# Kernel tuning notes

Measured on AMD Instinct MI355X. Metric: run time of the kernel, lower is better.

## Reference

```python
import jax, jax.numpy as jnp
import numpy as np

LATENT = 64
COND = 768
HEADS = 8
R = 8           # LoRA rank
SCALING = 1.0   # lora_alpha / r
SCALE = (LATENT / HEADS) ** -0.5


def _lora_linear(x, W, b, A, B):
    # loralib-style: y = x W^T + b + scaling * (x A^T) B^T
    return x @ W.T + b + SCALING * ((x @ A.T) @ B.T)


def setup_inputs() -> dict:
    key = jax.random.key(0)
    ks = jax.random.split(key, 20)
    B, C, H, W_ = 16, LATENT, 64, 64
    L = 77
    z = jax.random.normal(ks[0], (B, C, H, W_), dtype=jnp.float32)
    cond = jax.random.normal(ks[1], (B, L, COND), dtype=jnp.float32)

    def lin(k, out_d, in_d):
        k1, k2, k3 = jax.random.split(k, 3)
        W = jax.random.normal(k1, (out_d, in_d), dtype=jnp.float32) * 0.02
        b = jnp.zeros((out_d,), dtype=jnp.float32)
        A = jax.random.normal(k2, (R, in_d), dtype=jnp.float32) * 0.02
        Bm = jax.random.normal(k3, (out_d, R), dtype=jnp.float32) * 0.02
        return W, b, A, Bm

    Wq, bq, Aq, Bq = lin(ks[2], LATENT, LATENT)
    Wk, bk, Ak, Bk = lin(ks[3], LATENT, COND)
    Wv, bv, Av, Bv = lin(ks[4], LATENT, COND)
    Wo, bo, Ao, Bo = lin(ks[5], LATENT, LATENT)
    return dict(z=z, cond=cond,
                Wq=Wq, bq=bq, Aq=Aq, Bq=Bq,
                Wk=Wk, bk=bk, Ak=Ak, Bk=Bk,
                Wv=Wv, bv=bv, Av=Av, Bv=Bv,
                Wo=Wo, bo=bo, Ao=Ao, Bo=Bo)


def reference(z, cond, Wq, bq, Aq, Bq, Wk, bk, Ak, Bk, Wv, bv, Av, Bv, Wo, bo, Ao, Bo):
    B, C, H, W_ = z.shape
    hw = H * W_
    dh = C // HEADS
    z_flat = z.transpose(0, 2, 3, 1).reshape(B, hw, C)  # [B, hw, C]

    q = _lora_linear(z_flat, Wq, bq, Aq, Bq)   # [B, hw, C]
    k = _lora_linear(cond, Wk, bk, Ak, Bk)     # [B, L, C]
    v = _lora_linear(cond, Wv, bv, Av, Bv)     # [B, L, C]

    q = q.reshape(B, hw, HEADS, dh).transpose(0, 2, 1, 3)  # [B, h, hw, dh]
    k = k.reshape(B, -1, HEADS, dh).transpose(0, 2, 1, 3)  # [B, h, L, dh]
    v = v.reshape(B, -1, HEADS, dh).transpose(0, 2, 1, 3)

    dots = jnp.einsum('bhqd,bhkd->bhqk', q, k) * SCALE  # [B, h, hw, L]
    attn = jax.nn.softmax(dots, axis=-1)
    out = jnp.einsum('bhqk,bhkd->bhqd', attn, v)        # [B, h, hw, dh]
    out = out.transpose(0, 2, 1, 3).reshape(B, hw, C)
    out = _lora_linear(out, Wo, bo, Ao, Bo)
    return out.reshape(B, H, W_, C).transpose(0, 3, 1, 2)  # [B, C, H, W]
```

## Files before the change

### kernel.cpp

```cpp
#include <hip/hip_runtime.h>


#define HW   4096
#define CHN  64
#define LSEQ 77
#define CD   768
#define NB   16

#define OFF_WQ 0
#define OFF_WK 4096
#define OFF_WV 53248
#define OFF_WO 102400
#define OFF_K  106496
#define OFF_V  185344

#define QF 0.51011784563163f

__global__ __launch_bounds__(256) void prep_weights(
    const float* __restrict__ Wq, const float* __restrict__ Aq, const float* __restrict__ Bq,
    const float* __restrict__ Wk, const float* __restrict__ Ak, const float* __restrict__ Bk,
    const float* __restrict__ Wv, const float* __restrict__ Av, const float* __restrict__ Bv,
    const float* __restrict__ Wo, const float* __restrict__ Ao, const float* __restrict__ Bo,
    float* __restrict__ ws) {
  int idx = blockIdx.x * 256 + threadIdx.x;
  const float *W, *A, *Bm;
  float* out;
  int in_d, local;
  float scale = 1.0f;
  if (idx < 4096)        { W = Wq; A = Aq; Bm = Bq; out = ws + OFF_WQ; in_d = 64;  local = idx; scale = QF; }
  else if (idx < 53248)  { W = Wk; A = Ak; Bm = Bk; out = ws + OFF_WK; in_d = 768; local = idx - 4096; }
  else if (idx < 102400) { W = Wv; A = Av; Bm = Bv; out = ws + OFF_WV; in_d = 768; local = idx - 53248; }
  else                   { W = Wo; A = Ao; Bm = Bo; out = ws + OFF_WO; in_d = 64;  local = idx - 102400; }
  int co = local & 63;
  int c  = local >> 6;
  float val = W[co * in_d + c];
  #pragma unroll
  for (int r = 0; r < 8; r++) val += Bm[co * 8 + r] * A[r * in_d + c];
  out[local] = val * scale;
}

__global__ __launch_bounds__(512, 4) void kvproj2(
    const float* __restrict__ cond,
    const float* __restrict__ wkT,
    const float* __restrict__ wvT,
    const float* __restrict__ bk, const float* __restrict__ bv,
    float* __restrict__ kbuf,
    float* __restrict__ vbuf) {
  int kv = blockIdx.y;
  int t  = threadIdx.x;
  int w  = __builtin_amdgcn_readfirstlane(t >> 6);
  int co = t & 63;
  int row = blockIdx.x * 8 + w;
  const float* wT = kv ? wvT : wkT;
  const float* xr = cond + row * CD;
  float acc = (kv ? bv : bk)[co];
  #pragma unroll 8
  for (int c4 = 0; c4 < CD / 4; c4++) {
    float4 xv = *(const float4*)(xr + 4 * c4);
    acc = fmaf(xv.x, wT[(4 * c4 + 0) * 64 + co], acc);
    acc = fmaf(xv.y, wT[(4 * c4 + 1) * 64 + co], acc);
    acc = fmaf(xv.z, wT[(4 * c4 + 2) * 64 + co], acc);
    acc = fmaf(xv.w, wT[(4 * c4 + 3) * 64 + co], acc);
  }
  (kv ? vbuf : kbuf)[row * 64 + co] = acc;
}

__global__ __launch_bounds__(256, 2) void megattn(
    const float* __restrict__ z,
    const float* __restrict__ wqT,
    const float* __restrict__ bq,
    const float* __restrict__ kbuf,
    const float* __restrict__ vbuf,
    const float* __restrict__ woT,
    const float* __restrict__ bo,
    float* __restrict__ out) {
  __shared__ float smem[LSEQ * 64 * 2];
  int b  = blockIdx.y;
  int p0 = blockIdx.x * 128;
  int t  = threadIdx.x;
  int h  = t >> 5;
  int pl = t & 31;

  float* ks = smem;
  float* vs = smem + LSEQ * 64;
  {
    const float4* ksrc = (const float4*)(kbuf + b * LSEQ * 64);
    const float4* vsrc = (const float4*)(vbuf + b * LSEQ * 64);
    float4* kd = (float4*)ks;
    float4* vd = (float4*)vs;
    for (int i = t; i < LSEQ * 16; i += 256) { kd[i] = ksrc[i]; vd[i] = vsrc[i]; }
  }

  float qr[4][8];
  {
    const float4 b0 = *(const float4*)(bq + 8 * h);
    const float4 b1 = *(const float4*)(bq + 8 * h + 4);
    #pragma unroll
    for (int i = 0; i < 4; i++) {
      qr[i][0] = b0.x * QF; qr[i][1] = b0.y * QF; qr[i][2] = b0.z * QF; qr[i][3] = b0.w * QF;
      qr[i][4] = b1.x * QF; qr[i][5] = b1.y * QF; qr[i][6] = b1.z * QF; qr[i][7] = b1.w * QF;
    }
  }
  const float* zb = z + b * (CHN * HW) + p0 + pl;
  #pragma unroll 4
  for (int c = 0; c < 64; c++) {
    float4 w0 = *(const float4*)(wqT + c * 64 + 8 * h);
    float4 w1 = *(const float4*)(wqT + c * 64 + 8 * h + 4);
    float zv[4];
    #pragma unroll
    for (int i = 0; i < 4; i++) zv[i] = zb[c * HW + 32 * i];
    #pragma unroll
    for (int i = 0; i < 4; i++) {
      qr[i][0] = fmaf(zv[i], w0.x, qr[i][0]);
      qr[i][1] = fmaf(zv[i], w0.y, qr[i][1]);
      qr[i][2] = fmaf(zv[i], w0.z, qr[i][2]);
      qr[i][3] = fmaf(zv[i], w0.w, qr[i][3]);
      qr[i][4] = fmaf(zv[i], w1.x, qr[i][4]);
      qr[i][5] = fmaf(zv[i], w1.y, qr[i][5]);
      qr[i][6] = fmaf(zv[i], w1.z, qr[i][6]);
      qr[i][7] = fmaf(zv[i], w1.w, qr[i][7]);
    }
  }
  __syncthreads();

  float acc[4][8];
  float li[4];
  #pragma unroll
  for (int i = 0; i < 4; i++) {
    li[i] = 0.f;
    #pragma unroll
    for (int d = 0; d < 8; d++) acc[i][d] = 0.f;
  }
  #pragma unroll 2
  for (int j = 0; j < LSEQ; j++) {
    float4 k0 = *(const float4*)(ks + j * 64 + 8 * h);
    float4 k1 = *(const float4*)(ks + j * 64 + 8 * h + 4);
    float4 v0 = *(const float4*)(vs + j * 64 + 8 * h);
    float4 v1 = *(const float4*)(vs + j * 64 + 8 * h + 4);
    #pragma unroll
    for (int i = 0; i < 4; i++) {
      float s = qr[i][0] * k0.x;
      s = fmaf(qr[i][1], k0.y, s);
      s = fmaf(qr[i][2], k0.z, s);
      s = fmaf(qr[i][3], k0.w, s);
      s = fmaf(qr[i][4], k1.x, s);
      s = fmaf(qr[i][5], k1.y, s);
      s = fmaf(qr[i][6], k1.z, s);
      s = fmaf(qr[i][7], k1.w, s);
      float e = __builtin_amdgcn_exp2f(s);
      li[i] += e;
      acc[i][0] = fmaf(e, v0.x, acc[i][0]);
      acc[i][1] = fmaf(e, v0.y, acc[i][1]);
      acc[i][2] = fmaf(e, v0.z, acc[i][2]);
      acc[i][3] = fmaf(e, v0.w, acc[i][3]);
      acc[i][4] = fmaf(e, v1.x, acc[i][4]);
      acc[i][5] = fmaf(e, v1.y, acc[i][5]);
      acc[i][6] = fmaf(e, v1.z, acc[i][6]);
      acc[i][7] = fmaf(e, v1.w, acc[i][7]);
    }
  }
  __syncthreads();

  float* ao = smem;
  #pragma unroll
  for (int i = 0; i < 4; i++) {
    float inv = 1.0f / li[i];
    int p = pl + 32 * i;
    #pragma unroll
    for (int d = 0; d < 8; d++) ao[p * 65 + 8 * h + d] = acc[i][d] * inv;
  }
  __syncthreads();

  int q2 = t & 127;
  int chalf = __builtin_amdgcn_readfirstlane((t >> 7) & 1);
  float acc2[32];
  #pragma unroll
  for (int j2 = 0; j2 < 32; j2++) acc2[j2] = bo[chalf * 32 + j2];
  const float* aor = ao + q2 * 65;
  #pragma unroll 4
  for (int c = 0; c < 64; c++) {
    float xv = aor[c];
    const float* wr = woT + c * 64 + chalf * 32;
    #pragma unroll
    for (int j2 = 0; j2 < 32; j2++) acc2[j2] = fmaf(xv, wr[j2], acc2[j2]);
  }
  float* ob = out + b * (CHN * HW) + p0 + q2;
  #pragma unroll
  for (int j2 = 0; j2 < 32; j2++) ob[(chalf * 32 + j2) * HW] = acc2[j2];
}

extern "C" void kernel_launch(void* const* d_in, const int* in_sizes, int n_in,
                              void* d_out, int out_size, void* d_ws, size_t ws_size,
                              hipStream_t stream) {
  const float* z    = (const float*)d_in[0];
  const float* cond = (const float*)d_in[1];
  const float* Wq = (const float*)d_in[2];  const float* bq = (const float*)d_in[3];
  const float* Aq = (const float*)d_in[4];  const float* Bq = (const float*)d_in[5];
  const float* Wk = (const float*)d_in[6];  const float* bk = (const float*)d_in[7];
  const float* Ak = (const float*)d_in[8];  const float* Bk = (const float*)d_in[9];
  const float* Wv = (const float*)d_in[10]; const float* bv = (const float*)d_in[11];
  const float* Av = (const float*)d_in[12]; const float* Bv = (const float*)d_in[13];
  const float* Wo = (const float*)d_in[14]; const float* bo = (const float*)d_in[15];
  const float* Ao = (const float*)d_in[16]; const float* Bo = (const float*)d_in[17];
  float* ws  = (float*)d_ws;
  float* out = (float*)d_out;

  prep_weights<<<416, 256, 0, stream>>>(Wq, Aq, Bq, Wk, Ak, Bk, Wv, Av, Bv, Wo, Ao, Bo, ws);
  kvproj2<<<dim3(154, 2), 512, 0, stream>>>(cond, ws + OFF_WK, ws + OFF_WV, bk, bv,
                                            ws + OFF_K, ws + OFF_V);
  megattn<<<dim3(32, 16), 256, 0, stream>>>(z, ws + OFF_WQ, bq, ws + OFF_K, ws + OFF_V,
                                            ws + OFF_WO, bo, out);
}
```

Baseline: 169.0 us.

## Split K/V projection reduction across waves and reuse weights over four rows

The K/V projection kernel now stages four cond rows in shared memory and splits the 768-long reduction into four chunks, one per wave. Each thread loads a weight once and applies it to four rows, with a shared-memory reduction at the end. The intent is to cut redundant weight reads and shorten each thread's serial FMA chain, so more blocks run with more parallelism. The cost is extra shared memory, two barriers and a small reduction step.

```diff
diff --git a/kernel.cpp b/kernel.cpp
--- a/kernel.cpp
+++ b/kernel.cpp
@@ -39,30 +39,61 @@
   out[local] = val * scale;
 }
 
-__global__ __launch_bounds__(512, 4) void kvproj2(
+__global__ __launch_bounds__(256) void kvproj4(
     const float* __restrict__ cond,
     const float* __restrict__ wkT,
     const float* __restrict__ wvT,
     const float* __restrict__ bk, const float* __restrict__ bv,
     float* __restrict__ kbuf,
     float* __restrict__ vbuf) {
+  __shared__ float xs[4 * CD];
+  __shared__ float red[4][4][64];
   int kv = blockIdx.y;
+  int r0 = blockIdx.x * 4;
   int t  = threadIdx.x;
-  int w  = __builtin_amdgcn_readfirstlane(t >> 6);
   int co = t & 63;
-  int row = blockIdx.x * 8 + w;
-  const float* wT = kv ? wvT : wkT;
-  const float* xr = cond + row * CD;
-  float acc = (kv ? bv : bk)[co];
-  #pragma unroll 8
-  for (int c4 = 0; c4 < CD / 4; c4++) {
-    float4 xv = *(const float4*)(xr + 4 * c4);
-    acc = fmaf(xv.x, wT[(4 * c4 + 0) * 64 + co], acc);
-    acc = fmaf(xv.y, wT[(4 * c4 + 1) * 64 + co], acc);
-    acc = fmaf(xv.z, wT[(4 * c4 + 2) * 64 + co], acc);
-    acc = fmaf(xv.w, wT[(4 * c4 + 3) * 64 + co], acc);
-  }
-  (kv ? vbuf : kbuf)[row * 64 + co] = acc;
+  int q  = __builtin_amdgcn_readfirstlane(t >> 6);
+
+  {
+    const float4* src = (const float4*)(cond + r0 * CD);
+    float4* dst = (float4*)xs;
+    #pragma unroll
+    for (int i = 0; i < 3; i++) dst[t + 256 * i] = src[t + 256 * i];
+  }
+  __syncthreads();
+
+  const float* wT = (kv ? wvT : wkT) + q * 192 * 64 + co;
+  const float4* xs4 = (const float4*)xs;
+  float acc0 = 0.f, acc1 = 0.f, acc2 = 0.f, acc3 = 0.f;
+  #pragma unroll 4
+  for (int c4 = 0; c4 < 48; c4++) {
+    float w0 = wT[(4 * c4 + 0) * 64];
+    float w1 = wT[(4 * c4 + 1) * 64];
+    float w2 = wT[(4 * c4 + 2) * 64];
+    float w3 = wT[(4 * c4 + 3) * 64];
+    float4 x0 = xs4[0 * 192 + q * 48 + c4];
+    float4 x1 = xs4[1 * 192 + q * 48 + c4];
+    float4 x2 = xs4[2 * 192 + q * 48 + c4];
+    float4 x3 = xs4[3 * 192 + q * 48 + c4];
+    acc0 = fmaf(x0.x, w0, acc0); acc0 = fmaf(x0.y, w1, acc0);
+    acc0 = fmaf(x0.z, w2, acc0); acc0 = fmaf(x0.w, w3, acc0);
+    acc1 = fmaf(x1.x, w0, acc1); acc1 = fmaf(x1.y, w1, acc1);
+    acc1 = fmaf(x1.z, w2, acc1); acc1 = fmaf(x1.w, w3, acc1);
+    acc2 = fmaf(x2.x, w0, acc2); acc2 = fmaf(x2.y, w1, acc2);
+    acc2 = fmaf(x2.z, w2, acc2); acc2 = fmaf(x2.w, w3, acc2);
+    acc3 = fmaf(x3.x, w0, acc3); acc3 = fmaf(x3.y, w1, acc3);
+    acc3 = fmaf(x3.z, w2, acc3); acc3 = fmaf(x3.w, w3, acc3);
+  }
+  red[q][0][co] = acc0;
+  red[q][1][co] = acc1;
+  red[q][2][co] = acc2;
+  red[q][3][co] = acc3;
+  __syncthreads();
+
+  int lr = t >> 6;
+  float val = (kv ? bv : bk)[co]
+            + red[0][lr][co] + red[1][lr][co] + red[2][lr][co] + red[3][lr][co];
+  (kv ? vbuf : kbuf)[(r0 + lr) * 64 + co] = val;
 }
 
 __global__ __launch_bounds__(256, 2) void megattn(
@@ -206,7 +237,7 @@
   float* out = (float*)d_out;
 
   prep_weights<<<416, 256, 0, stream>>>(Wq, Aq, Bq, Wk, Ak, Bk, Wv, Av, Bv, Wo, Ao, Bo, ws);
-  kvproj2<<<dim3(154, 2), 512, 0, stream>>>(cond, ws + OFF_WK, ws + OFF_WV, bk, bv,
+  kvproj4<<<dim3(308, 2), 256, 0, stream>>>(cond, ws + OFF_WK, ws + OFF_WV, bk, bv,
                                             ws + OFF_K, ws + OFF_V);
   megattn<<<dim3(32, 16), 256, 0, stream>>>(z, ws + OFF_WQ, bq, ws + OFF_K, ws + OFF_V,
                                             ws + OFF_WO, bo, out);
```

Result: faster. 147.2 us (-12.9%).

## Split K/V projection reduction across waves with LDS partial-sum reduction

Applied to the files above, without the earlier changes.

Rewrites the K/V projection kernel so each block handles 4 rows, stages the condition rows in shared memory, and splits the 768-long reduction across 16 thread groups that each reuse a float4 weight load across four rows. Partial sums are combined through a shared-memory reduction before adding the bias. This targets the long serial dependency chain and per-thread scalar weight loads of the old one-row-per-wave kernel, and it adds block synchronisation and extra shared memory in exchange.

```diff
diff --git a/kernel.cpp b/kernel.cpp
--- a/kernel.cpp
+++ b/kernel.cpp
@@ -39,30 +39,68 @@
   out[local] = val * scale;
 }
 
-__global__ __launch_bounds__(512, 4) void kvproj2(
+__global__ __launch_bounds__(256) void kvproj5(
     const float* __restrict__ cond,
     const float* __restrict__ wkT,
     const float* __restrict__ wvT,
     const float* __restrict__ bk, const float* __restrict__ bv,
     float* __restrict__ kbuf,
     float* __restrict__ vbuf) {
+  __shared__ float xs[4 * CD];
+  __shared__ float red[16 * 256];
   int kv = blockIdx.y;
+  int r0 = blockIdx.x * 4;
   int t  = threadIdx.x;
-  int w  = __builtin_amdgcn_readfirstlane(t >> 6);
+  int l  = t & 63;
+  int q  = __builtin_amdgcn_readfirstlane(t >> 6);
+  int l16 = l & 15;
+  int cs  = l >> 4;
+
+  {
+    const float4* src = (const float4*)(cond + r0 * CD);
+    float4* dst = (float4*)xs;
+    #pragma unroll
+    for (int i = 0; i < 3; i++) dst[t + 256 * i] = src[t + 256 * i];
+  }
+  __syncthreads();
+
+  const float4* wT4 = (const float4*)(kv ? wvT : wkT);
+  float4 a0 = make_float4(0.f, 0.f, 0.f, 0.f);
+  float4 a1 = a0, a2 = a0, a3 = a0;
+  int cbase = q * 192 + cs;
+  #pragma unroll 8
+  for (int it = 0; it < 48; it++) {
+    int c = cbase + 4 * it;
+    float4 w  = wT4[c * 16 + l16];
+    float x0 = xs[0 * CD + c];
+    float x1 = xs[1 * CD + c];
+    float x2 = xs[2 * CD + c];
+    float x3 = xs[3 * CD + c];
+    a0.x = fmaf(x0, w.x, a0.x); a0.y = fmaf(x0, w.y, a0.y);
+    a0.z = fmaf(x0, w.z, a0.z); a0.w = fmaf(x0, w.w, a0.w);
+    a1.x = fmaf(x1, w.x, a1.x); a1.y = fmaf(x1, w.y, a1.y);
+    a1.z = fmaf(x1, w.z, a1.z); a1.w = fmaf(x1, w.w, a1.w);
+    a2.x = fmaf(x2, w.x, a2.x); a2.y = fmaf(x2, w.y, a2.y);
+    a2.z = fmaf(x2, w.z, a2.z); a2.w = fmaf(x2, w.w, a2.w);
+    a3.x = fmaf(x3, w.x, a3.x); a3.y = fmaf(x3, w.y, a3.y);
+    a3.z = fmaf(x3, w.z, a3.z); a3.w = fmaf(x3, w.w, a3.w);
+  }
+
+  {
+    float4* redq = (float4*)(red + (q * 4 + cs) * 256);
+    redq[0 * 16 + l16] = a0;
+    redq[1 * 16 + l16] = a1;
+    redq[2 * 16 + l16] = a2;
+    redq[3 * 16 + l16] = a3;
+  }
+  __syncthreads();
+
+  int r  = t >> 6;
   int co = t & 63;
-  int row = blockIdx.x * 8 + w;
-  const float* wT = kv ? wvT : wkT;
-  const float* xr = cond + row * CD;
-  float acc = (kv ? bv : bk)[co];
-  #pragma unroll 8
-  for (int c4 = 0; c4 < CD / 4; c4++) {
-    float4 xv = *(const float4*)(xr + 4 * c4);
-    acc = fmaf(xv.x, wT[(4 * c4 + 0) * 64 + co], acc);
-    acc = fmaf(xv.y, wT[(4 * c4 + 1) * 64 + co], acc);
-    acc = fmaf(xv.z, wT[(4 * c4 + 2) * 64 + co], acc);
-    acc = fmaf(xv.w, wT[(4 * c4 + 3) * 64 + co], acc);
-  }
-  (kv ? vbuf : kbuf)[row * 64 + co] = acc;
+  float val = (kv ? bv : bk)[co];
+  #pragma unroll
+  for (int g = 0; g < 16; g++) val += red[g * 256 + r * 64 + co];
+  (kv ? vbuf : kbuf)[(r0 + r) * 64 + co] = val;
 }
 
 __global__ __launch_bounds__(256, 2) void megattn(
@@ -206,7 +244,7 @@
   float* out = (float*)d_out;
 
   prep_weights<<<416, 256, 0, stream>>>(Wq, Aq, Bq, Wk, Ak, Bk, Wv, Av, Bv, Wo, Ao, Bo, ws);
-  kvproj2<<<dim3(154, 2), 512, 0, stream>>>(cond, ws + OFF_WK, ws + OFF_WV, bk, bv,
+  kvproj5<<<dim3(308, 2), 256, 0, stream>>>(cond, ws + OFF_WK, ws + OFF_WV, bk, bv,
                                             ws + OFF_K, ws + OFF_V);
   megattn<<<dim3(32, 16), 256, 0, stream>>>(z, ws + OFF_WQ, bq, ws + OFF_K, ws + OFF_V,
                                             ws + OFF_WO, bo, out);
```

Result: faster. 148.1 us (-12.3%).
